# Kernel optimization log

Hardware: AMD Instinct MI355X
Metric: run time of the kernel (lower is better)

## Reference

```python
import jax, jax.numpy as jnp
import numpy as np

STRIDE = 1  # stride3x3 init arg


def sparsemax(z):
    """Sparsemax along last axis (Martins & Astudillo 2016)."""
    K = z.shape[-1]
    zs = -jnp.sort(-z, axis=-1)                     # sorted descending
    cum = jnp.cumsum(zs, axis=-1)
    ks = jnp.arange(1, K + 1, dtype=z.dtype)
    support = (1 + ks * zs) > cum                   # [.., K] bool
    k_z = jnp.sum(support, axis=-1, keepdims=True)  # support size, int
    cum_k = jnp.take_along_axis(cum, k_z - 1, axis=-1)
    tau = (cum_k - 1) / k_z.astype(z.dtype)
    return jnp.maximum(z - tau, 0)


def setup_inputs() -> dict:
    key = jax.random.key(0)
    k1, k2, k3, k4 = jax.random.split(key, 4)
    B, Cin, Cout, H, W, K = 64, 512, 512, 28, 28, 8
    x = jax.random.normal(k1, (B, Cin, H, W), dtype=jnp.float32)
    gate_w = jax.random.normal(k2, (K, Cin), dtype=jnp.float32) * 0.02   # nn.Linear weight
    gate_b = jax.random.normal(k3, (K,), dtype=jnp.float32) * 0.02       # nn.Linear bias
    expert_w = jax.random.normal(k4, (K, Cout, Cin), dtype=jnp.float32) * 0.02  # K conv1x1 kernels (bias-free)
    return {"x": x, "gate_w": gate_w, "gate_b": gate_b, "expert_w": expert_w}


def reference(x, gate_w, gate_b, expert_w):
    # gate: sparsemax(Linear(mean_pool(x)))
    pooled = x.mean(axis=(2, 3))                         # [B, Cin]
    g = sparsemax(pooled @ gate_w.T + gate_b)            # [B, K], many exact zeros
    # sum_k g[b,k] * conv1x1_k(x) == conv1x1 with per-sample combined weight
    xs = x[:, :, ::STRIDE, ::STRIDE]                     # 1x1 conv with stride = subsample
    w_eff = jnp.einsum('bk,koi->boi', g, expert_w)       # [B, Cout, Cin]
    out = jnp.einsum('boi,bihw->bohw', w_eff, xs)        # [B, Cout, H', W']
    return out
```

## Files before the change

kernel.cpp:

```cpp
#include <hip/hip_runtime.h>

#define NB 64
#define CIN 512
#define COUT 512
#define HW 784
#define KEXP 8

typedef __attribute__((ext_vector_type(8))) short bf16x8;
typedef __attribute__((ext_vector_type(4))) float f32x4;

__device__ __forceinline__ unsigned f2bf1(float f) {
  unsigned u = __builtin_bit_cast(unsigned, f);
  return (u + 0x7FFFu + ((u >> 16) & 1u)) >> 16;
}
__device__ __forceinline__ unsigned f2bf2(float lo, float hi) {
  return f2bf1(lo) | (f2bf1(hi) << 16);
}

__global__ __launch_bounds__(256) void pool_kernel(const float* __restrict__ x,
                                                   float* __restrict__ pooled) {
  int w = threadIdx.x >> 6, lane = threadIdx.x & 63;
  int row = blockIdx.x * 4 + w;
  const float4* xr = (const float4*)(x + (size_t)row * HW);
  float s = 0.f;
  for (int i = lane; i < 196; i += 64) {
    float4 v = xr[i];
    s += (v.x + v.y) + (v.z + v.w);
  }
  #pragma unroll
  for (int off = 32; off; off >>= 1) s += __shfl_down(s, off);
  if (lane == 0) pooled[row] = s * (1.0f / 784.0f);
}

__global__ __launch_bounds__(256) void gate_kernel(const float* __restrict__ pooled,
                                                   const float* __restrict__ gw,
                                                   const float* __restrict__ gb,
                                                   float* __restrict__ g) {
  __shared__ float red[4][KEXP];
  int b = blockIdx.x;
  int t = threadIdx.x;
  int lane = t & 63, w = t >> 6;

  float p0 = pooled[b * CIN + t];
  float p1 = pooled[b * CIN + t + 256];
  float zk[KEXP];
  #pragma unroll
  for (int k = 0; k < KEXP; ++k)
    zk[k] = p0 * gw[k * CIN + t] + p1 * gw[k * CIN + t + 256];

  #pragma unroll
  for (int k = 0; k < KEXP; ++k) {
    float s = zk[k];
    #pragma unroll
    for (int off = 32; off; off >>= 1) s += __shfl_down(s, off);
    if (lane == 0) red[w][k] = s;
  }
  __syncthreads();

  if (t == 0) {
    float z[8], zs[8];
    #pragma unroll
    for (int j = 0; j < 8; ++j) {
      z[j] = (red[0][j] + red[1][j] + red[2][j] + red[3][j]) + gb[j];
      zs[j] = z[j];
    }
    #pragma unroll
    for (int a = 1; a < 8; ++a) {
      float v = zs[a]; int j = a;
      while (j > 0 && zs[j - 1] < v) { zs[j] = zs[j - 1]; --j; }
      zs[j] = v;
    }
    float cums[8]; float csum = 0.f;
    #pragma unroll
    for (int j = 0; j < 8; ++j) { csum += zs[j]; cums[j] = csum; }
    int kz = 0;
    #pragma unroll
    for (int j = 0; j < 8; ++j)
      if (1.0f + (float)(j + 1) * zs[j] > cums[j]) kz = j + 1;
    float tau = (cums[kz - 1] - 1.0f) / (float)kz;
    #pragma unroll
    for (int j = 0; j < 8; ++j) g[b * 8 + j] = fmaxf(z[j] - tau, 0.0f);
  }
}

__global__ __launch_bounds__(256) void weff_kernel(const float* __restrict__ E,
                                                   const float* __restrict__ g,
                                                   uint4* __restrict__ wt) {
  __shared__ float gs[NB * KEXP];
  int t = threadIdx.x;
  ((float2*)gs)[t] = ((const float2*)g)[t];
  int o = blockIdx.x * 16 + (t & 15);
  int i = blockIdx.y * 128 + (t >> 4) * 8;
  int b0 = blockIdx.z * 32;
  float e[8][8];
  #pragma unroll
  for (int k = 0; k < 8; ++k) {
    const float4* p = (const float4*)(E + (size_t)k * (COUT * CIN) + (size_t)o * CIN + i);
    float4 a = p[0], c = p[1];
    e[k][0] = a.x; e[k][1] = a.y; e[k][2] = a.z; e[k][3] = a.w;
    e[k][4] = c.x; e[k][5] = c.y; e[k][6] = c.z; e[k][7] = c.w;
  }
  __syncthreads();
  int base = ((o >> 8) * 16 + (i >> 5)) * 1024 + ((i >> 3) & 3) * 256 + (o & 255);
  for (int b = b0; b < b0 + 32; ++b) {
    float acc[8] = {0, 0, 0, 0, 0, 0, 0, 0};
    #pragma unroll
    for (int k = 0; k < 8; ++k) {
      float gv = gs[b * 8 + k];
      #pragma unroll
      for (int j = 0; j < 8; ++j) acc[j] += gv * e[k][j];
    }
    uint4 pk;
    pk.x = f2bf2(acc[0], acc[1]); pk.y = f2bf2(acc[2], acc[3]);
    pk.z = f2bf2(acc[4], acc[5]); pk.w = f2bf2(acc[6], acc[7]);
    wt[(size_t)base + (size_t)b * 32768] = pk;
  }
}

__global__ __launch_bounds__(512) void gemm_kernel(const uint4* __restrict__ weff,
                                                   const float* __restrict__ x,
                                                   float* __restrict__ out) {
  __shared__ uint4 ldsB[2][448];
  int id = blockIdx.x;
  int xcd = id & 7, s = id >> 3;
  int bloc = s / 14, inner = s - bloc * 14;
  int b = xcd * 8 + bloc;
  int mb = inner & 1, nb = inner >> 1;

  int t = threadIdx.x;
  int lane = t & 63, w = t >> 6;
  int l15 = lane & 15, l4 = lane >> 4;

  const uint4* asrc = weff + (size_t)b * 32768 + (size_t)mb * 16384
                      + l4 * 256 + w * 32 + l15;
  int u = t;
  int kgrp = u / 112, col = u - kgrp * 112;
  const float* xp = x + (size_t)b * (CIN * HW) + (size_t)kgrp * 8 * HW
                    + (size_t)nb * 112 + col;
  int uswz = u ^ ((u >> 3) & 7);

  f32x4 acc[2][7] = {};
  uint4 a2[2][2];
  float Bv[2][8];

  if (w < 7) {
    #pragma unroll
    for (int j = 0; j < 8; ++j) Bv[0][j] = xp[(size_t)j * HW];
  }
  a2[0][0] = asrc[0];
  a2[0][1] = asrc[16];

  #pragma unroll
  for (int kk = 0; kk < 16; ++kk) {
    if (w < 7) {
      uint4 pk;
      pk.x = f2bf2(Bv[kk & 1][0], Bv[kk & 1][1]);
      pk.y = f2bf2(Bv[kk & 1][2], Bv[kk & 1][3]);
      pk.z = f2bf2(Bv[kk & 1][4], Bv[kk & 1][5]);
      pk.w = f2bf2(Bv[kk & 1][6], Bv[kk & 1][7]);
      ldsB[kk & 1][uswz] = pk;
    }
    if (kk < 15) {
      if (w < 7) {
        #pragma unroll
        for (int j = 0; j < 8; ++j)
          Bv[(kk + 1) & 1][j] = xp[(size_t)(kk + 1) * 32 * HW + (size_t)j * HW];
      }
      a2[(kk + 1) & 1][0] = asrc[(kk + 1) * 1024];
      a2[(kk + 1) & 1][1] = asrc[(kk + 1) * 1024 + 16];
    }

    asm volatile("s_waitcnt lgkmcnt(0)" ::: "memory");
    __builtin_amdgcn_s_barrier();
    __builtin_amdgcn_sched_barrier(0);

    bf16x8 af0 = __builtin_bit_cast(bf16x8, a2[kk & 1][0]);
    bf16x8 af1 = __builtin_bit_cast(bf16x8, a2[kk & 1][1]);
    #pragma unroll
    for (int uu = 0; uu < 7; ++uu) {
      int un = l4 * 112 + uu * 16 + l15;
      bf16x8 bf = *(const bf16x8*)&ldsB[kk & 1][un ^ ((un >> 3) & 7)];
      acc[0][uu] = __builtin_amdgcn_mfma_f32_16x16x32_bf16(af0, bf, acc[0][uu], 0, 0, 0);
      acc[1][uu] = __builtin_amdgcn_mfma_f32_16x16x32_bf16(af1, bf, acc[1][uu], 0, 0, 0);
    }
  }

  int orow0 = mb * 256 + w * 32 + l4 * 4;
  int ocol = nb * 112 + l15;
  #pragma unroll
  for (int m = 0; m < 2; ++m) {
    #pragma unroll
    for (int uu = 0; uu < 7; ++uu) {
      float* op = out + ((size_t)b * COUT + orow0 + m * 16) * HW + ocol + uu * 16;
      #pragma unroll
      for (int r = 0; r < 4; ++r) op[(size_t)r * HW] = acc[m][uu][r];
    }
  }
}

extern "C" void kernel_launch(void* const* d_in, const int* in_sizes, int n_in,
                              void* d_out, int out_size, void* d_ws, size_t ws_size,
                              hipStream_t stream) {
  const float* x        = (const float*)d_in[0];
  const float* gate_w   = (const float*)d_in[1];
  const float* gate_b   = (const float*)d_in[2];
  const float* expert_w = (const float*)d_in[3];
  float* out = (float*)d_out;

  char* ws = (char*)d_ws;
  uint4* weff   = (uint4*)ws;
  float* pooled = (float*)(ws + 33554432);
  float* g      = (float*)(ws + 33554432 + 131072);

  pool_kernel<<<8192, 256, 0, stream>>>(x, pooled);
  gate_kernel<<<NB, 256, 0, stream>>>(pooled, gate_w, gate_b, g);
  weff_kernel<<<dim3(32, 4, 2), 256, 0, stream>>>(expert_w, g, weff);
  gemm_kernel<<<896, 512, 0, stream>>>(weff, x, out);
}
```

Before: 82.06 us.

## Process two K-slices per barrier stage in GEMM main loop

Restructures the GEMM main loop so each stage converts and stores two 32-channel K slices to both LDS buffers at once, then runs MFMAs on both, with a second barrier closing the stage. Global prefetches run two slices ahead. This halves the number of barrier-separated stages and lengthens the compute run between synchronisations. In exchange it holds more prefetched registers in flight and adds a trailing barrier per stage. The LDS write/read phases also no longer overlap.

```diff
diff --git a/kernel.cpp b/kernel.cpp
--- a/kernel.cpp
+++ b/kernel.cpp
@@ -146,43 +146,74 @@
   if (w < 7) {
     #pragma unroll
     for (int j = 0; j < 8; ++j) Bv[0][j] = xp[(size_t)j * HW];
+    #pragma unroll
+    for (int j = 0; j < 8; ++j) Bv[1][j] = xp[(size_t)32 * HW + (size_t)j * HW];
   }
   a2[0][0] = asrc[0];
   a2[0][1] = asrc[16];
-
-  #pragma unroll
-  for (int kk = 0; kk < 16; ++kk) {
+  a2[1][0] = asrc[1024];
+  a2[1][1] = asrc[1024 + 16];
+
+  #pragma unroll
+  for (int S = 0; S < 8; ++S) {
+    const int k0 = 2 * S, k1 = 2 * S + 1;
+
     if (w < 7) {
       uint4 pk;
-      pk.x = f2bf2(Bv[kk & 1][0], Bv[kk & 1][1]);
-      pk.y = f2bf2(Bv[kk & 1][2], Bv[kk & 1][3]);
-      pk.z = f2bf2(Bv[kk & 1][4], Bv[kk & 1][5]);
-      pk.w = f2bf2(Bv[kk & 1][6], Bv[kk & 1][7]);
-      ldsB[kk & 1][uswz] = pk;
-    }
-    if (kk < 15) {
-      if (w < 7) {
+      pk.x = f2bf2(Bv[0][0], Bv[0][1]); pk.y = f2bf2(Bv[0][2], Bv[0][3]);
+      pk.z = f2bf2(Bv[0][4], Bv[0][5]); pk.w = f2bf2(Bv[0][6], Bv[0][7]);
+      ldsB[0][uswz] = pk;
+      uint4 qk;
+      qk.x = f2bf2(Bv[1][0], Bv[1][1]); qk.y = f2bf2(Bv[1][2], Bv[1][3]);
+      qk.z = f2bf2(Bv[1][4], Bv[1][5]); qk.w = f2bf2(Bv[1][6], Bv[1][7]);
+      ldsB[1][uswz] = qk;
+      if (S < 7) {
         #pragma unroll
         for (int j = 0; j < 8; ++j)
-          Bv[(kk + 1) & 1][j] = xp[(size_t)(kk + 1) * 32 * HW + (size_t)j * HW];
-      }
-      a2[(kk + 1) & 1][0] = asrc[(kk + 1) * 1024];
-      a2[(kk + 1) & 1][1] = asrc[(kk + 1) * 1024 + 16];
+          Bv[0][j] = xp[(size_t)(k0 + 2) * 32 * HW + (size_t)j * HW];
+        #pragma unroll
+        for (int j = 0; j < 8; ++j)
+          Bv[1][j] = xp[(size_t)(k1 + 2) * 32 * HW + (size_t)j * HW];
+      }
     }
 
     asm volatile("s_waitcnt lgkmcnt(0)" ::: "memory");
     __builtin_amdgcn_s_barrier();
     __builtin_amdgcn_sched_barrier(0);
 
-    bf16x8 af0 = __builtin_bit_cast(bf16x8, a2[kk & 1][0]);
-    bf16x8 af1 = __builtin_bit_cast(bf16x8, a2[kk & 1][1]);
-    #pragma unroll
-    for (int uu = 0; uu < 7; ++uu) {
-      int un = l4 * 112 + uu * 16 + l15;
-      bf16x8 bf = *(const bf16x8*)&ldsB[kk & 1][un ^ ((un >> 3) & 7)];
-      acc[0][uu] = __builtin_amdgcn_mfma_f32_16x16x32_bf16(af0, bf, acc[0][uu], 0, 0, 0);
-      acc[1][uu] = __builtin_amdgcn_mfma_f32_16x16x32_bf16(af1, bf, acc[1][uu], 0, 0, 0);
-    }
+    {
+      bf16x8 af0 = __builtin_bit_cast(bf16x8, a2[0][0]);
+      bf16x8 af1 = __builtin_bit_cast(bf16x8, a2[0][1]);
+      #pragma unroll
+      for (int uu = 0; uu < 7; ++uu) {
+        int un = l4 * 112 + uu * 16 + l15;
+        bf16x8 bf = *(const bf16x8*)&ldsB[0][un ^ ((un >> 3) & 7)];
+        acc[0][uu] = __builtin_amdgcn_mfma_f32_16x16x32_bf16(af0, bf, acc[0][uu], 0, 0, 0);
+        acc[1][uu] = __builtin_amdgcn_mfma_f32_16x16x32_bf16(af1, bf, acc[1][uu], 0, 0, 0);
+      }
+      if (S < 7) {
+        a2[0][0] = asrc[(k0 + 2) * 1024];
+        a2[0][1] = asrc[(k0 + 2) * 1024 + 16];
+      }
+    }
+    {
+      bf16x8 af0 = __builtin_bit_cast(bf16x8, a2[1][0]);
+      bf16x8 af1 = __builtin_bit_cast(bf16x8, a2[1][1]);
+      #pragma unroll
+      for (int uu = 0; uu < 7; ++uu) {
+        int un = l4 * 112 + uu * 16 + l15;
+        bf16x8 bf = *(const bf16x8*)&ldsB[1][un ^ ((un >> 3) & 7)];
+        acc[0][uu] = __builtin_amdgcn_mfma_f32_16x16x32_bf16(af0, bf, acc[0][uu], 0, 0, 0);
+        acc[1][uu] = __builtin_amdgcn_mfma_f32_16x16x32_bf16(af1, bf, acc[1][uu], 0, 0, 0);
+      }
+      if (S < 7) {
+        a2[1][0] = asrc[(k1 + 2) * 1024];
+        a2[1][1] = asrc[(k1 + 2) * 1024 + 16];
+      }
+    }
+
+    __builtin_amdgcn_s_barrier();
+    __builtin_amdgcn_sched_barrier(0);
   }
 
   int orow0 = mb * 256 + w * 32 + l4 * 4;
```

Result: slower. 98.65 us (+20.2%).
